# Performance work log

Measured on AMD Instinct MI355X. Metric: run time of the kernel, lower is better.

## Reference

```python
import jax, jax.numpy as jnp
import numpy as np

K = 16          # nsample
EPS = 1e-5      # BatchNorm eps
NEG_SLOPE = 0.1 # LeakyReLU slope


def _knn_gather(pc2, pc1, feat2, k):
    """pc2 [B,N2,3], pc1 [B,N1,3], feat2 [B,N2,C] ->
       neighbor_xyz [B,N1,k,3], neighbor_feat [B,N1,k,C] (k nearest in pc2 per pc1 point)."""
    # squared euclidean distances (monotone in cdist, same topk indices)
    d2 = (jnp.sum(pc1 * pc1, -1)[:, :, None]
          - 2.0 * jnp.einsum('bic,bjc->bij', pc1, pc2)
          + jnp.sum(pc2 * pc2, -1)[:, None, :])
    idx = jax.lax.top_k(-d2, k)[1]            # [B,N1,k] smallest distances
    gather = jax.vmap(lambda pts, i: pts[i])  # batch-wise fancy gather
    return gather(pc2, idx), gather(feat2, idx)


def _weightnet(xyz, W1, b1, gamma, beta, mean, var, W2, b2):
    """xyz [B,N,K,3] -> [B,N,K,C_out]; Conv2d(1x1)->BN(eval)->ReLU->Conv2d(1x1)."""
    h = jnp.einsum('bnkc,oc->bnko', xyz, W1) + b1
    h = gamma * (h - mean) * jax.lax.rsqrt(var + EPS) + beta
    h = jax.nn.relu(h)
    return jnp.einsum('bnkc,oc->bnko', h, W2) + b2


def _correlator(pc1, pc2, feature1, feature2, mlp_params, wn1, wn2):
    pc1_t = pc1.transpose(0, 2, 1)   # [B,N,3]
    pc2_t = pc2.transpose(0, 2, 1)
    f1 = feature1.transpose(0, 2, 1) # [B,N,C]
    f2 = feature2.transpose(0, 2, 1)
    # Stage 1: point-to-patch cost volume
    nbr_xyz, nbr_f2 = _knn_gather(pc2_t, pc1_t, f2, K)
    direction = nbr_xyz - pc1_t[:, :, None, :]                     # [B,N,K,3]
    f1e = jnp.broadcast_to(f1[:, :, None, :], nbr_f2.shape[:3] + (f1.shape[-1],))
    x = jnp.concatenate([f1e, nbr_f2, direction], axis=-1)         # [B,N,K,2C+3]
    for W, b in mlp_params:
        x = jax.nn.leaky_relu(jnp.einsum('bnkc,oc->bnko', x, W) + b, NEG_SLOPE)
    w1 = _weightnet(direction, *wn1)
    x = jnp.sum(w1 * x, axis=2)                                    # [B,N,C]
    # Stage 2: patch-to-patch self aggregation in pc1 space
    nbr_xyz2, nbr_self = _knn_gather(pc1_t, pc1_t, x, K)
    direction2 = nbr_xyz2 - pc1_t[:, :, None, :]
    w2 = _weightnet(direction2, *wn2)
    out = jnp.sum(w2 * nbr_self, axis=2)                           # [B,N,C]
    return out.transpose(0, 2, 1)                                  # [B,C,N]


def setup_inputs() -> dict:
    key = jax.random.key(0)
    ks = jax.random.split(key, 24)
    B, N, C = 2, 4096, 256
    inc = 2 * C + 3  # 515
    nrm = lambda k, s, sc: (jax.random.normal(k, s, dtype=jnp.float32) * sc)
    uni = lambda k, s: jax.random.uniform(k, s, dtype=jnp.float32, minval=0.5, maxval=1.5)
    return {
        'pc1': nrm(ks[0], (B, 3, N), 1.0),
        'pc2': nrm(ks[1], (B, 3, N), 1.0),
        'feature1': nrm(ks[2], (B, C, N), 1.0),
        'feature2': nrm(ks[3], (B, C, N), 1.0),
        # MLP 1x1 conv stack
        'W0': nrm(ks[4], (C, inc), 0.05), 'b0': jnp.zeros((C,), jnp.float32),
        'W1': nrm(ks[5], (C, C), 0.05),  'b1': jnp.zeros((C,), jnp.float32),
        'W2': nrm(ks[6], (C, C), 0.05),  'b2': jnp.zeros((C,), jnp.float32),
        # WeightNet 1 (3->8->C)
        'wn1_W1': nrm(ks[7], (8, 3), 0.5), 'wn1_b1': jnp.zeros((8,), jnp.float32),
        'wn1_gamma': uni(ks[8], (8,)), 'wn1_beta': nrm(ks[9], (8,), 0.1),
        'wn1_mean': nrm(ks[10], (8,), 0.1), 'wn1_var': uni(ks[11], (8,)),
        'wn1_W2': nrm(ks[12], (C, 8), 0.1), 'wn1_b2': jnp.zeros((C,), jnp.float32),
        # WeightNet 2
        'wn2_W1': nrm(ks[13], (8, 3), 0.5), 'wn2_b1': jnp.zeros((8,), jnp.float32),
        'wn2_gamma': uni(ks[14], (8,)), 'wn2_beta': nrm(ks[15], (8,), 0.1),
        'wn2_mean': nrm(ks[16], (8,), 0.1), 'wn2_var': uni(ks[17], (8,)),
        'wn2_W2': nrm(ks[18], (C, 8), 0.1), 'wn2_b2': jnp.zeros((C,), jnp.float32),
    }


def reference(pc1, pc2, feature1, feature2,
              W0, b0, W1, b1, W2, b2,
              wn1_W1, wn1_b1, wn1_gamma, wn1_beta, wn1_mean, wn1_var, wn1_W2, wn1_b2,
              wn2_W1, wn2_b1, wn2_gamma, wn2_beta, wn2_mean, wn2_var, wn2_W2, wn2_b2):
    mlp_params = [(W0, b0), (W1, b1), (W2, b2)]
    wn1 = (wn1_W1, wn1_b1, wn1_gamma, wn1_beta, wn1_mean, wn1_var, wn1_W2, wn1_b2)
    wn2 = (wn2_W1, wn2_b1, wn2_gamma, wn2_beta, wn2_mean, wn2_var, wn2_W2, wn2_b2)
    return _correlator(pc1, pc2, feature1, feature2, mlp_params, wn1, wn2)
```

## Files before the change

### kernel.cpp

```cpp
#include <hip/hip_runtime.h>
#include <math.h>

#define KNB 16
#define NPTS 4096
#define NB 2
#define CH 256
#define BNEPS 1e-5f

#define MTOT (NB * NPTS * KNB)
#define BM 128

typedef short bf16x8 __attribute__((ext_vector_type(8)));
typedef float f32x4 __attribute__((ext_vector_type(4)));

__device__ __forceinline__ unsigned short f2bf(float x) {
  unsigned u = __float_as_uint(x);
  return (unsigned short)((u + 0x7fffu + ((u >> 16) & 1u)) >> 16);
}
__device__ __forceinline__ float bf2f(unsigned short h) {
  return __uint_as_float(((unsigned)h) << 16);
}

#define GLOAD_LDS16(g, l)                                                     \
  __builtin_amdgcn_global_load_lds(                                           \
      (const __attribute__((address_space(1))) unsigned int*)(g),             \
      (__attribute__((address_space(3))) unsigned int*)(l), 16, 0, 0)

__global__ __launch_bounds__(256) void pack2_pts(const float* __restrict__ pc1,
                                                 const float* __restrict__ pc2,
                                                 float4* __restrict__ pk1,
                                                 float4* __restrict__ pk2) {
  int id = blockIdx.x * 256 + threadIdx.x;
  const float* in = (id < 8192) ? pc1 : pc2;
  float4* out = (id < 8192) ? pk1 : pk2;
  int q = id & 8191;
  int b = q >> 12, n = q & 4095;
  const float* pb = in + (size_t)b * 3 * NPTS;
  float x = pb[n], y = pb[NPTS + n], z = pb[2 * NPTS + n];
  float nn = __fadd_rn(__fadd_rn(__fmul_rn(x, x), __fmul_rn(y, y)), __fmul_rn(z, z));
  out[q] = make_float4(x, y, z, nn);
}

__global__ __launch_bounds__(256) void knn3c_kernel(const float4* __restrict__ pk1,
                                                    const float4* __restrict__ pk2,
                                                    int* __restrict__ idx1,
                                                    int* __restrict__ idx2) {
  __shared__ unsigned short sarr[4][4096];
  __shared__ unsigned long long surv[4][128];
  const int wid = threadIdx.x >> 6;
  const int lane = threadIdx.x & 63;
  const int gw = blockIdx.x * 4 + wid;
  const int which = gw >> 13;
  const int qi = gw & 8191;
  const int b = qi >> 12;
  const float4* pts = (which ? pk1 : pk2) + ((size_t)b << 12);
  float4 qp = pk1[qi];
  const float qx = qp.x, qy = qp.y, qz = qp.z, qn = qp.w;
  unsigned short* S = sarr[wid];

  unsigned int mymin = 0xFFFFu;
#pragma unroll 8
  for (int it = 0; it < 64; ++it) {
    int j = (it << 6) + lane;
    float4 pt = pts[j];
    float dot = __fadd_rn(__fadd_rn(__fmul_rn(qx, pt.x), __fmul_rn(qy, pt.y)),
                          __fmul_rn(qz, pt.z));
    float d = __fadd_rn(__fsub_rn(qn, __fmul_rn(2.f, dot)), pt.w);
    unsigned int u = __float_as_uint(d);
    unsigned int s = u ^ (unsigned int)(((int)u >> 31) | (int)0x80000000);
    unsigned int k16 = s >> 16;
    S[j] = (unsigned short)k16;
    mymin = mymin < k16 ? mymin : k16;
  }

  unsigned int v = mymin;
#pragma unroll
  for (int k = 2; k <= 64; k <<= 1) {
#pragma unroll
    for (int jj = k >> 1; jj >= 1; jj >>= 1) {
      unsigned int o = (unsigned int)__shfl_xor((int)v, jj);
      bool up = ((lane & k) == 0);
      bool low = ((lane & jj) == 0);
      bool tmin = (up == low);
      unsigned int mn = v < o ? v : o;
      unsigned int mx = v < o ? o : v;
      v = tmin ? mn : mx;
    }
  }

  unsigned long long* SV = surv[wid];
  unsigned int thr = (unsigned int)__shfl((int)v, 15);
  int base = 0;
  for (int attempt = 0; attempt < 2; ++attempt) {
    SV[lane] = ~0ull;
    SV[64 + lane] = ~0ull;
    base = 0;
    for (int it = 0; it < 64; ++it) {
      int j = (it << 6) + lane;
      bool hit = (unsigned int)S[j] <= thr;
      unsigned long long m = __ballot(hit);
      if (m) {
        float4 pt = pts[j];
        float dot = __fadd_rn(__fadd_rn(__fmul_rn(qx, pt.x), __fmul_rn(qy, pt.y)),
                              __fmul_rn(qz, pt.z));
        float d = __fadd_rn(__fsub_rn(qn, __fmul_rn(2.f, dot)), pt.w);
        unsigned int u = __float_as_uint(d);
        unsigned int s = u ^ (unsigned int)(((int)u >> 31) | (int)0x80000000);
        int r = base + (int)__popcll(m & ((1ull << lane) - 1ull));
        if (hit && r < 128) SV[r] = ((unsigned long long)s << 32) | (unsigned int)j;
        base += (int)__popcll(m);
      }
    }
    if (base <= 128) break;
    if (attempt == 0) {
      int idx = 23, cnt = 0, tries = 0;
      for (;;) {
        thr = (unsigned int)__shfl((int)v, idx);
        cnt = 0;
        for (int it = 0; it < 64; ++it) {
          unsigned long long m = __ballot((unsigned int)S[(it << 6) + lane] <= thr);
          cnt += __popcll(m);
        }
        if ((cnt >= 16 && cnt <= 128) || ++tries >= 6) break;
        if (cnt < 16) idx = (idx + 12 > 63) ? 63 : idx + 12;
        else idx = (idx - 8 < 0) ? 0 : idx - 8;
      }
    }
  }
  unsigned long long k0 = SV[lane];
  unsigned long long k1 = SV[64 + lane];

#pragma unroll
  for (int k = 2; k <= 128; k <<= 1) {
#pragma unroll
    for (int jj = k >> 1; jj >= 1; jj >>= 1) {
      if (jj == 64) {
        unsigned long long a = k0 < k1 ? k0 : k1;
        unsigned long long c = k0 < k1 ? k1 : k0;
        k0 = a; k1 = c;
      } else {
        {
          unsigned long long o = __shfl_xor(k0, jj);
          bool up = ((lane & k) == 0);
          bool low = ((lane & jj) == 0);
          bool tmin = (up == low);
          unsigned long long mn = k0 < o ? k0 : o;
          unsigned long long mx = k0 < o ? o : k0;
          k0 = tmin ? mn : mx;
        }
        {
          unsigned long long o = __shfl_xor(k1, jj);
          int e = 64 + lane;
          bool up = ((e & k) == 0);
          bool low = ((lane & jj) == 0);
          bool tmin = (up == low);
          unsigned long long mn = k1 < o ? k1 : o;
          unsigned long long mx = k1 < o ? o : k1;
          k1 = tmin ? mn : mx;
        }
      }
    }
  }

  int* op = (which ? idx2 : idx1) + (size_t)qi * KNB;
  if (lane < 16) op[lane] = (int)(k0 & 0xFFFFFFFFu);
}

__global__ __launch_bounds__(256) void conv_feat2(const float* __restrict__ f1,
                                                  const float* __restrict__ f2,
                                                  unsigned short* __restrict__ f1b,
                                                  unsigned short* __restrict__ f2b) {
  int gid = blockIdx.x;
  const float* in = (gid < 8192) ? f1 : f2;
  unsigned short* out = (gid < 8192) ? f1b : f2b;
  int bn = gid & 8191;
  int b = bn >> 12, n = bn & 4095;
  int c = threadIdx.x;
  out[(size_t)bn * CH + c] = f2bf(in[((size_t)(b * CH + c)) * NPTS + n]);
}

__global__ __launch_bounds__(256) void conv_w2(const float* __restrict__ W0,
                                               const float* __restrict__ W1,
                                               const float* __restrict__ W2,
                                               unsigned short* __restrict__ W0a,
                                               unsigned short* __restrict__ W0bp,
                                               unsigned short* __restrict__ W1b,
                                               unsigned short* __restrict__ W2b) {
  int r = blockIdx.x, c = threadIdx.x;
  if (r < 256) {
    W0a[r * 256 + c] = f2bf(W0[(size_t)r * 515 + c]);
    W0bp[r * 256 + c] = f2bf(W0[(size_t)r * 515 + 256 + c]);
  } else if (r < 512) {
    int rr = r - 256;
    W1b[rr * 256 + c] = f2bf(W1[rr * 256 + c]);
  } else {
    int rr = r - 512;
    W2b[rr * 256 + c] = f2bf(W2[rr * 256 + c]);
  }
}

__global__ __launch_bounds__(512) void small_gemm(
    const unsigned short* __restrict__ f1b, const unsigned short* __restrict__ f2b,
    const unsigned short* __restrict__ W0a, const unsigned short* __restrict__ W0bp,
    const float* __restrict__ b0, float* __restrict__ g1, float* __restrict__ G2) {
  __shared__ char smem[8192 + 16384];
  const int tid = threadIdx.x;
  const int lane = tid & 63;
  const int w = tid >> 6;
  const int wm = w >> 2, wn = w & 3;
  const bool isG2 = blockIdx.x >= 64;
  const int m0 = (blockIdx.x & 63) * BM;
  const unsigned short* Asrc = isG2 ? f2b : f1b;
  const unsigned short* Wb = isG2 ? W0bp : W0a;
  float* dst = isG2 ? G2 : g1;

  f32x4 acc[4][4];
#pragma unroll
  for (int nf = 0; nf < 4; ++nf) {
    float bv = isG2 ? 0.f : b0[wn * 64 + nf * 16 + (lane & 15)];
#pragma unroll
    for (int mf = 0; mf < 4; ++mf) acc[mf][nf] = (f32x4){bv, bv, bv, bv};
  }

  const int ar = tid >> 2;
  const int aql = (tid & 3) ^ ((ar >> 1) & 3);
  const int am = m0 + ar;
  const int br0 = tid >> 2;
  const int bq0 = (tid & 3) ^ ((br0 >> 1) & 3);
  const int br1 = (tid + 512) >> 2;
  const int bq1 = (tid & 3) ^ ((br1 >> 1) & 3);

  char* AsW = smem + (w << 10);
  char* BsW0 = smem + 8192 + (w << 10);
  char* BsW1 = smem + 8192 + 8192 + (w << 10);

  for (int kc = 0; kc < 8; ++kc) {
    __syncthreads();
    GLOAD_LDS16(Asrc + ((size_t)am << 8) + kc * 32 + aql * 8, AsW);
    GLOAD_LDS16(Wb + (size_t)br0 * 256 + kc * 32 + bq0 * 8, BsW0);
    GLOAD_LDS16(Wb + (size_t)br1 * 256 + kc * 32 + bq1 * 8, BsW1);
    __syncthreads();

    bf16x8 af[4], bfr[4];
#pragma unroll
    for (int mf = 0; mf < 4; ++mf) {
      int r = wm * 64 + mf * 16 + (lane & 15);
      int off = r * 64 + ((((lane >> 4)) ^ ((r >> 1) & 3)) << 4);
      af[mf] = *(const bf16x8*)(smem + off);
    }
#pragma unroll
    for (int nf = 0; nf < 4; ++nf) {
      int r = wn * 64 + nf * 16 + (lane & 15);
      int off = r * 64 + ((((lane >> 4)) ^ ((r >> 1) & 3)) << 4);
      bfr[nf] = *(const bf16x8*)(smem + 8192 + off);
    }
#pragma unroll
    for (int mf = 0; mf < 4; ++mf)
#pragma unroll
      for (int nf = 0; nf < 4; ++nf)
        acc[mf][nf] = __builtin_amdgcn_mfma_f32_16x16x32_bf16(af[mf], bfr[nf], acc[mf][nf], 0, 0, 0);
  }

#pragma unroll
  for (int mf = 0; mf < 4; ++mf) {
#pragma unroll
    for (int nf = 0; nf < 4; ++nf) {
      int n = wn * 64 + nf * 16 + (lane & 15);
#pragma unroll
      for (int j = 0; j < 4; ++j) {
        int m = m0 + wm * 64 + mf * 16 + (lane >> 4) * 4 + j;
        dst[(size_t)m * 256 + n] = acc[mf][nf][j];
      }
    }
  }
}

__global__ __launch_bounds__(256) void combine_kernel(
    const float* __restrict__ g1, const float* __restrict__ G2,
    const float* __restrict__ W0,
    const float* __restrict__ pc1, const float* __restrict__ pc2,
    const int* __restrict__ idx1,
    const float* __restrict__ wW1, const float* __restrict__ wb1,
    const float* __restrict__ wg, const float* __restrict__ wbe,
    const float* __restrict__ wmn, const float* __restrict__ wv,
    unsigned short* __restrict__ h1, float* __restrict__ h1wn) {
  __shared__ int nbrs[KNB];
  __shared__ float dirs[KNB][4];
  int bn = blockIdx.x;
  int b = bn >> 12, n = bn & 4095;
  int t = threadIdx.x;
  if (t < KNB) nbrs[t] = idx1[(size_t)bn * KNB + t];
  __syncthreads();
  if (t < 128) {
    int k = t >> 3, jj = t & 7;
    int j = nbrs[k];
    const float* p1 = pc1 + (size_t)b * 3 * NPTS;
    const float* p2 = pc2 + (size_t)b * 3 * NPTS;
    float d0 = p2[j] - p1[n];
    float d1 = p2[NPTS + j] - p1[NPTS + n];
    float d2 = p2[2 * NPTS + j] - p1[2 * NPTS + n];
    if (jj == 0) { dirs[k][0] = d0; dirs[k][1] = d1; dirs[k][2] = d2; }
    float hv = wb1[jj];
    hv = fmaf(d0, wW1[jj * 3], hv);
    hv = fmaf(d1, wW1[jj * 3 + 1], hv);
    hv = fmaf(d2, wW1[jj * 3 + 2], hv);
    hv = wg[jj] * (hv - wmn[jj]) * (1.f / sqrtf(wv[jj] + BNEPS)) + wbe[jj];
    h1wn[(size_t)(bn * KNB + k) * 8 + jj] = fmaxf(hv, 0.f);
  }
  __syncthreads();
  int c = t;
  float g1v = g1[((size_t)bn << 8) + c];
  float wc0 = W0[(size_t)c * 515 + 512];
  float wc1 = W0[(size_t)c * 515 + 513];
  float wc2 = W0[(size_t)c * 515 + 514];
  const float* G2b = G2 + (((size_t)b << 12) << 8);
  unsigned short* hp = h1 + ((size_t)bn * KNB) * 256 + c;
#pragma unroll
  for (int k = 0; k < KNB; ++k) {
    float s = g1v + G2b[((size_t)nbrs[k] << 8) + c];
    s = fmaf(dirs[k][0], wc0, s);
    s = fmaf(dirs[k][1], wc1, s);
    s = fmaf(dirs[k][2], wc2, s);
    s = s >= 0.f ? s : 0.1f * s;
    hp[k * 256] = f2bf(s);
  }
}

__global__ __launch_bounds__(512) void gemm256(
    const unsigned short* __restrict__ Asrc, const unsigned short* __restrict__ Wb,
    const float* __restrict__ bias, unsigned short* __restrict__ dst) {
  __shared__ char smem[8192 + 16384];
  const int tid = threadIdx.x;
  const int lane = tid & 63;
  const int w = tid >> 6;
  const int wm = w >> 2, wn = w & 3;
  const int m0 = blockIdx.x * BM;

  f32x4 acc[4][4];
#pragma unroll
  for (int nf = 0; nf < 4; ++nf) {
    float bv = bias[wn * 64 + nf * 16 + (lane & 15)];
#pragma unroll
    for (int mf = 0; mf < 4; ++mf) acc[mf][nf] = (f32x4){bv, bv, bv, bv};
  }

  const int ar = tid >> 2;
  const int aql = (tid & 3) ^ ((ar >> 1) & 3);
  const int am = m0 + ar;
  const int br0 = tid >> 2;
  const int bq0 = (tid & 3) ^ ((br0 >> 1) & 3);
  const int br1 = (tid + 512) >> 2;
  const int bq1 = (tid & 3) ^ ((br1 >> 1) & 3);

  char* AsW = smem + (w << 10);
  char* BsW0 = smem + 8192 + (w << 10);
  char* BsW1 = smem + 8192 + 8192 + (w << 10);

  for (int kc = 0; kc < 8; ++kc) {
    __syncthreads();
    GLOAD_LDS16(Asrc + ((size_t)am << 8) + kc * 32 + aql * 8, AsW);
    GLOAD_LDS16(Wb + (size_t)br0 * 256 + kc * 32 + bq0 * 8, BsW0);
    GLOAD_LDS16(Wb + (size_t)br1 * 256 + kc * 32 + bq1 * 8, BsW1);
    __syncthreads();

    bf16x8 af[4], bfr[4];
#pragma unroll
    for (int mf = 0; mf < 4; ++mf) {
      int r = wm * 64 + mf * 16 + (lane & 15);
      int off = r * 64 + ((((lane >> 4)) ^ ((r >> 1) & 3)) << 4);
      af[mf] = *(const bf16x8*)(smem + off);
    }
#pragma unroll
    for (int nf = 0; nf < 4; ++nf) {
      int r = wn * 64 + nf * 16 + (lane & 15);
      int off = r * 64 + ((((lane >> 4)) ^ ((r >> 1) & 3)) << 4);
      bfr[nf] = *(const bf16x8*)(smem + 8192 + off);
    }
#pragma unroll
    for (int mf = 0; mf < 4; ++mf)
#pragma unroll
      for (int nf = 0; nf < 4; ++nf)
        acc[mf][nf] = __builtin_amdgcn_mfma_f32_16x16x32_bf16(af[mf], bfr[nf], acc[mf][nf], 0, 0, 0);
  }

#pragma unroll
  for (int mf = 0; mf < 4; ++mf) {
#pragma unroll
    for (int nf = 0; nf < 4; ++nf) {
      int n = wn * 64 + nf * 16 + (lane & 15);
#pragma unroll
      for (int j = 0; j < 4; ++j) {
        int m = m0 + wm * 64 + mf * 16 + (lane >> 4) * 4 + j;
        float v = acc[mf][nf][j];
        v = v >= 0.f ? v : 0.1f * v;
        dst[(size_t)m * 256 + n] = f2bf(v);
      }
    }
  }
}

__global__ __launch_bounds__(256) void wreduce_kernel(
    const unsigned short* __restrict__ h2, const float* __restrict__ h1wn,
    const float* __restrict__ wW2, const float* __restrict__ wb2,
    float* __restrict__ out1) {
  __shared__ float g[KNB][8];
  int bn = blockIdx.x;
  int t = threadIdx.x;
  if (t < 128) g[t >> 3][t & 7] = h1wn[(size_t)(bn * KNB + (t >> 3)) * 8 + (t & 7)];
  float wrow[8];
#pragma unroll
  for (int jj = 0; jj < 8; ++jj) wrow[jj] = wW2[t * 8 + jj];
  float wb = wb2[t];
  __syncthreads();
  float o = 0.f;
#pragma unroll
  for (int k = 0; k < KNB; ++k) {
    float w1 = wb;
#pragma unroll
    for (int jj = 0; jj < 8; ++jj) w1 = fmaf(g[k][jj], wrow[jj], w1);
    float v = bf2f(h2[(size_t)(bn * KNB + k) * 256 + t]);
    o = fmaf(w1, v, o);
  }
  out1[(size_t)bn * 256 + t] = o;
}

__global__ __launch_bounds__(256) void stage2_kernel(
    const float* __restrict__ out1, const float* __restrict__ pc1,
    const int* __restrict__ idx2,
    const float* __restrict__ wn_W1, const float* __restrict__ wn_b1,
    const float* __restrict__ wn_g, const float* __restrict__ wn_be,
    const float* __restrict__ wn_m, const float* __restrict__ wn_v,
    const float* __restrict__ wn_W2, const float* __restrict__ wn_b2,
    float* __restrict__ outp) {
  __shared__ float h1[KNB][8];
  __shared__ int nbrs[KNB];
  int bn = blockIdx.x;
  int b = bn >> 12, n = bn & 4095;
  int t = threadIdx.x;
  if (t < KNB) nbrs[t] = idx2[(size_t)bn * KNB + t];
  __syncthreads();
  if (t < 128) {
    int k = t >> 3, jj = t & 7;
    int j = nbrs[k];
    const float* p1 = pc1 + (size_t)b * 3 * NPTS;
    float d0 = p1[j] - p1[n];
    float d1 = p1[NPTS + j] - p1[NPTS + n];
    float d2v = p1[2 * NPTS + j] - p1[2 * NPTS + n];
    float hv = d0 * wn_W1[jj * 3] + d1 * wn_W1[jj * 3 + 1] + d2v * wn_W1[jj * 3 + 2] + wn_b1[jj];
    hv = wn_g[jj] * (hv - wn_m[jj]) * (1.f / sqrtf(wn_v[jj] + BNEPS)) + wn_be[jj];
    h1[k][jj] = fmaxf(hv, 0.f);
  }
  __syncthreads();
  float wrow[8];
#pragma unroll
  for (int jj = 0; jj < 8; ++jj) wrow[jj] = wn_W2[t * 8 + jj];
  float wb = wn_b2[t];
  float outv = 0.f;
#pragma unroll
  for (int k = 0; k < KNB; ++k) {
    float w2 = wb;
#pragma unroll
    for (int jj = 0; jj < 8; ++jj) w2 = fmaf(h1[k][jj], wrow[jj], w2);
    float v = out1[((size_t)(b * NPTS) + nbrs[k]) * CH + t];
    outv = fmaf(w2, v, outv);
  }
  outp[((size_t)(b * CH) + t) * NPTS + n] = outv;
}

extern "C" void kernel_launch(void* const* d_in, const int* in_sizes, int n_in,
                              void* d_out, int out_size, void* d_ws, size_t ws_size,
                              hipStream_t stream) {
  const float* pc1 = (const float*)d_in[0];
  const float* pc2 = (const float*)d_in[1];
  const float* f1 = (const float*)d_in[2];
  const float* f2 = (const float*)d_in[3];
  const float* W0 = (const float*)d_in[4];
  const float* b0 = (const float*)d_in[5];
  const float* W1 = (const float*)d_in[6];
  const float* b1 = (const float*)d_in[7];
  const float* W2 = (const float*)d_in[8];
  const float* b2 = (const float*)d_in[9];
  const float* wn1_W1 = (const float*)d_in[10];
  const float* wn1_b1 = (const float*)d_in[11];
  const float* wn1_g = (const float*)d_in[12];
  const float* wn1_be = (const float*)d_in[13];
  const float* wn1_m = (const float*)d_in[14];
  const float* wn1_v = (const float*)d_in[15];
  const float* wn1_W2 = (const float*)d_in[16];
  const float* wn1_b2 = (const float*)d_in[17];
  const float* wn2_W1 = (const float*)d_in[18];
  const float* wn2_b1 = (const float*)d_in[19];
  const float* wn2_g = (const float*)d_in[20];
  const float* wn2_be = (const float*)d_in[21];
  const float* wn2_m = (const float*)d_in[22];
  const float* wn2_v = (const float*)d_in[23];
  const float* wn2_W2 = (const float*)d_in[24];
  const float* wn2_b2 = (const float*)d_in[25];

  unsigned short* f1b = (unsigned short*)d_ws;
  unsigned short* f2b = f1b + (size_t)NB * NPTS * CH;
  unsigned short* W0a = f2b + (size_t)NB * NPTS * CH;
  unsigned short* W0bp = W0a + (size_t)256 * 256;
  unsigned short* W1b = W0bp + (size_t)256 * 256;
  unsigned short* W2b = W1b + (size_t)256 * 256;
  unsigned short* h = W2b + (size_t)256 * 256;
  float* g1 = (float*)(h + (size_t)MTOT * 256);
  float* G2 = g1 + (size_t)NB * NPTS * CH;
  float* h1wn = G2 + (size_t)NB * NPTS * CH;
  float* out1 = h1wn + (size_t)MTOT * 8;
  int* idx1 = (int*)(out1 + (size_t)NB * NPTS * CH);
  int* idx2 = idx1 + (size_t)MTOT;
  float4* pk1 = (float4*)(idx2 + (size_t)MTOT);
  float4* pk2 = pk1 + (size_t)NB * NPTS;

  pack2_pts<<<NB * NPTS * 2 / 256, 256, 0, stream>>>(pc1, pc2, pk1, pk2);
  knn3c_kernel<<<NB * NPTS * 2 / 4, 256, 0, stream>>>(pk1, pk2, idx1, idx2);
  conv_feat2<<<NB * NPTS * 2, 256, 0, stream>>>(f1, f2, f1b, f2b);
  conv_w2<<<768, 256, 0, stream>>>(W0, W1, W2, W0a, W0bp, W1b, W2b);
  small_gemm<<<128, 512, 0, stream>>>(f1b, f2b, W0a, W0bp, b0, g1, G2);
  combine_kernel<<<NB * NPTS, 256, 0, stream>>>(
      g1, G2, W0, pc1, pc2, idx1, wn1_W1, wn1_b1, wn1_g, wn1_be, wn1_m, wn1_v,
      h, h1wn);
  gemm256<<<MTOT / BM, 512, 0, stream>>>(h, W1b, b1, h);
  gemm256<<<MTOT / BM, 512, 0, stream>>>(h, W2b, b2, h);
  wreduce_kernel<<<NB * NPTS, 256, 0, stream>>>(h, h1wn, wn1_W2, wn1_b2, out1);
  stage2_kernel<<<NB * NPTS, 256, 0, stream>>>(
      out1, pc1, idx2, wn2_W1, wn2_b1, wn2_g, wn2_be, wn2_m, wn2_v, wn2_W2, wn2_b2,
      (float*)d_out);
}
```

Baseline: 261.9 us.

## Fuse weightnet-weighted neighbor reduction into final MLP GEMM epilogue

Result: faster. 248.5 us, median of 3 (-5.1%).

```diff
diff --git a/kernel.cpp b/kernel.cpp
--- a/kernel.cpp
+++ b/kernel.cpp
@@ -399,29 +399,101 @@
   }
 }
 
-__global__ __launch_bounds__(256) void wreduce_kernel(
-    const unsigned short* __restrict__ h2, const float* __restrict__ h1wn,
+__global__ __launch_bounds__(512) void gemm256_wred(
+    const unsigned short* __restrict__ Asrc, const unsigned short* __restrict__ Wb,
+    const float* __restrict__ bias, const float* __restrict__ h1wn,
     const float* __restrict__ wW2, const float* __restrict__ wb2,
     float* __restrict__ out1) {
-  __shared__ float g[KNB][8];
-  int bn = blockIdx.x;
-  int t = threadIdx.x;
-  if (t < 128) g[t >> 3][t & 7] = h1wn[(size_t)(bn * KNB + (t >> 3)) * 8 + (t & 7)];
-  float wrow[8];
-#pragma unroll
-  for (int jj = 0; jj < 8; ++jj) wrow[jj] = wW2[t * 8 + jj];
-  float wb = wb2[t];
-  __syncthreads();
-  float o = 0.f;
-#pragma unroll
-  for (int k = 0; k < KNB; ++k) {
-    float w1 = wb;
-#pragma unroll
-    for (int jj = 0; jj < 8; ++jj) w1 = fmaf(g[k][jj], wrow[jj], w1);
-    float v = bf2f(h2[(size_t)(bn * KNB + k) * 256 + t]);
-    o = fmaf(w1, v, o);
-  }
-  out1[(size_t)bn * 256 + t] = o;
+  __shared__ char smem[8192 + 16384];
+  __shared__ float hw[1024];
+  const int tid = threadIdx.x;
+  const int lane = tid & 63;
+  const int w = tid >> 6;
+  const int wm = w >> 2, wn = w & 3;
+  const int m0 = blockIdx.x * BM;
+
+  hw[tid] = h1wn[(size_t)blockIdx.x * 1024 + tid];
+  hw[tid + 512] = h1wn[(size_t)blockIdx.x * 1024 + 512 + tid];
+
+  f32x4 acc[4][4];
+#pragma unroll
+  for (int nf = 0; nf < 4; ++nf) {
+    float bv = bias[wn * 64 + nf * 16 + (lane & 15)];
+#pragma unroll
+    for (int mf = 0; mf < 4; ++mf) acc[mf][nf] = (f32x4){bv, bv, bv, bv};
+  }
+
+  const int ar = tid >> 2;
+  const int aql = (tid & 3) ^ ((ar >> 1) & 3);
+  const int am = m0 + ar;
+  const int br0 = tid >> 2;
+  const int bq0 = (tid & 3) ^ ((br0 >> 1) & 3);
+  const int br1 = (tid + 512) >> 2;
+  const int bq1 = (tid & 3) ^ ((br1 >> 1) & 3);
+
+  char* AsW = smem + (w << 10);
+  char* BsW0 = smem + 8192 + (w << 10);
+  char* BsW1 = smem + 8192 + 8192 + (w << 10);
+
+  for (int kc = 0; kc < 8; ++kc) {
+    __syncthreads();
+    GLOAD_LDS16(Asrc + ((size_t)am << 8) + kc * 32 + aql * 8, AsW);
+    GLOAD_LDS16(Wb + (size_t)br0 * 256 + kc * 32 + bq0 * 8, BsW0);
+    GLOAD_LDS16(Wb + (size_t)br1 * 256 + kc * 32 + bq1 * 8, BsW1);
+    __syncthreads();
+
+    bf16x8 af[4], bfr[4];
+#pragma unroll
+    for (int mf = 0; mf < 4; ++mf) {
+      int r = wm * 64 + mf * 16 + (lane & 15);
+      int off = r * 64 + ((((lane >> 4)) ^ ((r >> 1) & 3)) << 4);
+      af[mf] = *(const bf16x8*)(smem + off);
+    }
+#pragma unroll
+    for (int nf = 0; nf < 4; ++nf) {
+      int r = wn * 64 + nf * 16 + (lane & 15);
+      int off = r * 64 + ((((lane >> 4)) ^ ((r >> 1) & 3)) << 4);
+      bfr[nf] = *(const bf16x8*)(smem + 8192 + off);
+    }
+#pragma unroll
+    for (int mf = 0; mf < 4; ++mf)
+#pragma unroll
+      for (int nf = 0; nf < 4; ++nf)
+        acc[mf][nf] = __builtin_amdgcn_mfma_f32_16x16x32_bf16(af[mf], bfr[nf], acc[mf][nf], 0, 0, 0);
+  }
+
+#pragma unroll
+  for (int nf = 0; nf < 4; ++nf) {
+    int n = wn * 64 + nf * 16 + (lane & 15);
+    float wbv = wb2[n];
+    float wr[8];
+#pragma unroll
+    for (int jj = 0; jj < 8; ++jj) wr[jj] = wW2[n * 8 + jj];
+#pragma unroll
+    for (int mf = 0; mf < 4; ++mf) {
+      int bnL = wm * 4 + mf;
+      float part = 0.f;
+#pragma unroll
+      for (int j = 0; j < 4; ++j) {
+        int k = (lane >> 4) * 4 + j;
+        const float4* hp = (const float4*)&hw[(bnL * 16 + k) * 8];
+        float4 ha = hp[0], hb = hp[1];
+        float w1 = wbv;
+        w1 = fmaf(ha.x, wr[0], w1); w1 = fmaf(ha.y, wr[1], w1);
+        w1 = fmaf(ha.z, wr[2], w1); w1 = fmaf(ha.w, wr[3], w1);
+        w1 = fmaf(hb.x, wr[4], w1); w1 = fmaf(hb.y, wr[5], w1);
+        w1 = fmaf(hb.z, wr[6], w1); w1 = fmaf(hb.w, wr[7], w1);
+        float v = acc[mf][nf][j];
+        v = v >= 0.f ? v : 0.1f * v;
+        v = bf2f(f2bf(v));
+        part = fmaf(w1, v, part);
+      }
+      part += __shfl_xor(part, 16);
+      part += __shfl_xor(part, 32);
+      if (lane < 16)
+        out1[(size_t)(blockIdx.x * 8 + bnL) * 256 + n] = part;
+    }
+  }
 }
 
 __global__ __launch_bounds__(256) void stage2_kernel(
@@ -522,8 +594,7 @@
       g1, G2, W0, pc1, pc2, idx1, wn1_W1, wn1_b1, wn1_g, wn1_be, wn1_m, wn1_v,
       h, h1wn);
   gemm256<<<MTOT / BM, 512, 0, stream>>>(h, W1b, b1, h);
-  gemm256<<<MTOT / BM, 512, 0, stream>>>(h, W2b, b2, h);
-  wreduce_kernel<<<NB * NPTS, 256, 0, stream>>>(h, h1wn, wn1_W2, wn1_b2, out1);
+  gemm256_wred<<<MTOT / BM, 512, 0, stream>>>(h, W2b, b2, h1wn, wn1_W2, wn1_b2, out1);
   stage2_kernel<<<NB * NPTS, 256, 0, stream>>>(
       out1, pc1, idx2, wn2_W1, wn2_b1, wn2_g, wn2_be, wn2_m, wn2_v, wn2_W2, wn2_b2,
       (float*)d_out);
```
